# Optimization experiments

Measured on AMD Instinct MI355X. Metric: run time of the kernel, lower is better.

## Reference

```python
import jax, jax.numpy as jnp
import numpy as np

D_MODEL = 768
NUM_HEADS = 12
D_K = D_MODEL // NUM_HEADS


def setup_inputs() -> dict:
    key = jax.random.key(0)
    ks = jax.random.split(key, 11)
    B, S = 2, 2048
    scale = 1.0 / np.sqrt(D_MODEL)
    inp = {
        'query': jax.random.normal(ks[0], (B, S, D_MODEL), jnp.float32),
        'key': jax.random.normal(ks[1], (B, S, D_MODEL), jnp.float32),
        'value': jax.random.normal(ks[2], (B, S, D_MODEL), jnp.float32),
        # Linear params (torch nn.Linear: y = x @ W.T + b); store as [in,out]
        'Wq': jax.random.normal(ks[3], (D_MODEL, D_MODEL), jnp.float32) * scale,
        'bq': jnp.zeros((D_MODEL,), jnp.float32),
        'Wk': jax.random.normal(ks[4], (D_MODEL, D_MODEL), jnp.float32) * scale,
        'bk': jnp.zeros((D_MODEL,), jnp.float32),
        'Wv': jax.random.normal(ks[5], (D_MODEL, D_MODEL), jnp.float32) * scale,
        'bv': jnp.zeros((D_MODEL,), jnp.float32),
        'Wo': jax.random.normal(ks[6], (D_MODEL, D_MODEL), jnp.float32) * scale,
        'bo': jnp.zeros((D_MODEL,), jnp.float32),
    }
    return inp


def _split_heads(x):
    B, S, _ = x.shape
    return x.reshape(B, S, NUM_HEADS, D_K).transpose(0, 2, 1, 3)  # [B,H,S,d_k]


def reference(query, key, value, Wq, bq, Wk, bk, Wv, bv, Wo, bo):
    q = _split_heads(query @ Wq + bq)
    k = _split_heads(key @ Wk + bk)
    v = _split_heads(value @ Wv + bv)
    scores = jnp.einsum('bhqd,bhkd->bhqk', q, k) / np.sqrt(D_K)  # [B,H,S,S]
    attn = jax.nn.softmax(scores, axis=-1)
    x = jnp.einsum('bhqk,bhkd->bhqd', attn, v)  # [B,H,S,d_k]
    B, H, S, _ = x.shape
    x = x.transpose(0, 2, 1, 3).reshape(B, S, D_MODEL)
    return x @ Wo + bo
```

## Files before the change

kernel.cpp:

```cpp
#include <hip/hip_runtime.h>
#include <hip/hip_bf16.h>

#define DM     768
#define HEADS  12
#define DK     64
#define SQ     2048
#define BATCH  2
#define ROWS   4096
#define KTILES 24

typedef __attribute__((ext_vector_type(4))) float f32x4;
typedef __bf16 bf16x8 __attribute__((ext_vector_type(8)));
typedef unsigned short u16x8 __attribute__((ext_vector_type(8)));

#define QSCALE 0.180336880f

static __device__ __forceinline__ unsigned short f2bf(float f) {
    union { float f; unsigned u; } v; v.f = f;
    unsigned u = v.u;
    unsigned lsb = (u >> 16) & 1u;
    u += 0x7fffu + lsb;
    return (unsigned short)(u >> 16);
}

static __device__ __forceinline__ unsigned pack_bf16(float a, float b) {
    __hip_bfloat162 h = __float22bfloat162_rn(make_float2(a, b));
    unsigned u;
    __builtin_memcpy(&u, &h, 4);
    return u;
}

static __device__ __forceinline__ float fexp2(float x) {
#if __has_builtin(__builtin_amdgcn_exp2f)
    return __builtin_amdgcn_exp2f(x);
#else
    return exp2f(x);
#endif
}

static __device__ __forceinline__ bf16x8 load_bf16x8(const unsigned short* p) {
    u16x8 u = *(const u16x8*)p;
    return __builtin_bit_cast(bf16x8, u);
}

static __device__ __forceinline__ void gld_lds16(const unsigned short* g, unsigned short* l) {
    __builtin_amdgcn_global_load_lds((const __attribute__((address_space(1))) void*)g,
                                     (__attribute__((address_space(3))) void*)l,
                                     16, 0, 0);
}

static __device__ __forceinline__ void drain_dma() {
    asm volatile("s_waitcnt vmcnt(0)" ::: "memory");
}

__global__ __launch_bounds__(256) void cvt_frag3(const float* __restrict__ X0,
                                                 const float* __restrict__ X1,
                                                 const float* __restrict__ X2,
                                                 unsigned short* __restrict__ A0,
                                                 unsigned short* __restrict__ A1,
                                                 unsigned short* __restrict__ A2) {
    int z = blockIdx.z;
    const float* X = z == 0 ? X0 : z == 1 ? X1 : X2;
    unsigned short* A = z == 0 ? A0 : z == 1 ? A1 : A2;
    int p = blockIdx.x * 256 + threadIdx.x;
    int lane = p & 63;
    int g = p >> 6;
    int ks = g % KTILES;
    int mt = g / KTILES;
    int row = mt * 16 + (lane & 15);
    int k   = ks * 32 + (lane >> 4) * 8;
    const float* src = X + (size_t)row * DM + k;
    float4 v0 = *(const float4*)src;
    float4 v1 = *(const float4*)(src + 4);
    u16x8 o;
    o[0]=f2bf(v0.x); o[1]=f2bf(v0.y); o[2]=f2bf(v0.z); o[3]=f2bf(v0.w);
    o[4]=f2bf(v1.x); o[5]=f2bf(v1.y); o[6]=f2bf(v1.z); o[7]=f2bf(v1.w);
    *(u16x8*)(A + (size_t)p * 8) = o;
}

__global__ __launch_bounds__(256) void wt_frag4(const float* __restrict__ W0,
                                                const float* __restrict__ W1,
                                                const float* __restrict__ W2,
                                                const float* __restrict__ W3,
                                                unsigned short* __restrict__ F0,
                                                unsigned short* __restrict__ F1,
                                                unsigned short* __restrict__ F2,
                                                unsigned short* __restrict__ F3) {
    int z = blockIdx.z;
    const float* W = z == 0 ? W0 : z == 1 ? W1 : z == 2 ? W2 : W3;
    unsigned short* F = z == 0 ? F0 : z == 1 ? F1 : z == 2 ? F2 : F3;
    int p = blockIdx.x * 256 + threadIdx.x;
    int lane = p & 63;
    int t = (p >> 6) & 3;
    int g = p >> 8;
    int ks = g % KTILES;
    int nb = g / KTILES;
    int n = nb * 64 + t * 16 + (lane & 15);
    int k = ks * 32 + (lane >> 4) * 8;
    u16x8 o;
#pragma unroll
    for (int j = 0; j < 8; ++j) o[j] = f2bf(W[(size_t)(k + j) * DM + n]);
    *(u16x8*)(F + (size_t)p * 8) = o;
}

__global__ __launch_bounds__(256) void gemm_qkv(const unsigned short* __restrict__ A0,
                                                const unsigned short* __restrict__ A1,
                                                const unsigned short* __restrict__ A2,
                                                const unsigned short* __restrict__ F0,
                                                const unsigned short* __restrict__ F1,
                                                const unsigned short* __restrict__ F2,
                                                const float* __restrict__ b0,
                                                const float* __restrict__ b1,
                                                const float* __restrict__ b2,
                                                unsigned short* __restrict__ Qo,
                                                unsigned short* __restrict__ Ko,
                                                unsigned short* __restrict__ Vo) {
    __shared__ __align__(16) unsigned short ldsB[2][8192];

    int z = blockIdx.z;
    const unsigned short* A = z == 0 ? A0 : z == 1 ? A1 : A2;
    const unsigned short* F = z == 0 ? F0 : z == 1 ? F1 : F2;
    const float* bias        = z == 0 ? b0 : z == 1 ? b1 : b2;

    int w    = threadIdx.x >> 6;
    int lane = threadIdx.x & 63;
    int l15  = lane & 15;
    int quad = lane >> 4;
    int m0 = blockIdx.y * 128 + w * 32;
    int nb = blockIdx.x;
    int mt0 = m0 >> 4;

    const unsigned short* Ap = A + (size_t)mt0 * KTILES * 512 + lane * 8;
    const unsigned short* Bsrc = F + (size_t)nb * KTILES * 4 * 512 + w * 2048 + lane * 8;
    unsigned short* Bdst = &ldsB[0][w * 2048];

    f32x4 acc[2][4];
#pragma unroll
    for (int i = 0; i < 2; ++i)
#pragma unroll
        for (int t = 0; t < 4; ++t) acc[i][t] = (f32x4){0.f, 0.f, 0.f, 0.f};

#define BSTAGE(buf, c) do { \
        _Pragma("unroll") \
        for (int j = 0; j < 4; ++j) \
            gld_lds16(Bsrc + (size_t)(c) * 8192 + j * 512, Bdst + (buf) * 8192 + j * 512); \
    } while (0)

    BSTAGE(0, 0);

    bf16x8 a_cur[2][4];
#pragma unroll
    for (int k4 = 0; k4 < 4; ++k4)
#pragma unroll
        for (int i = 0; i < 2; ++i)
            a_cur[i][k4] = load_bf16x8(Ap + ((size_t)i * KTILES + k4) * 512);

    for (int c = 0; c < 6; ++c) {
        drain_dma();
        __syncthreads();
        if (c < 5) BSTAGE((c + 1) & 1, c + 1);
        const unsigned short* Bl = &ldsB[c & 1][0];
#pragma unroll
        for (int k4 = 0; k4 < 4; ++k4) {
#pragma unroll
            for (int t = 0; t < 4; ++t) {
                bf16x8 bb = load_bf16x8(Bl + (k4 * 4 + t) * 512 + lane * 8);
#pragma unroll
                for (int i = 0; i < 2; ++i)
                    acc[i][t] = __builtin_amdgcn_mfma_f32_16x16x32_bf16(a_cur[i][k4], bb, acc[i][t], 0, 0, 0);
            }
            if (c < 5) {
#pragma unroll
                for (int i = 0; i < 2; ++i)
                    a_cur[i][k4] = load_bf16x8(Ap + ((size_t)i * KTILES + (c + 1) * 4 + k4) * 512);
            }
        }
    }
#undef BSTAGE

    float scale = (z == 0) ? QSCALE : 1.0f;
#pragma unroll
    for (int t = 0; t < 4; ++t) {
        int col = nb * 64 + t * 16 + l15;
        float bv = bias[col];
        int h = col >> 6, d = col & (DK - 1);
#pragma unroll
        for (int i = 0; i < 2; ++i)
#pragma unroll
            for (int r = 0; r < 4; ++r) {
                int row = m0 + i * 16 + quad * 4 + r;
                float v = (acc[i][t][r] + bv) * scale;
                int bb = row >> 11, s = row & (SQ - 1);
                size_t bh = (size_t)(bb * HEADS + h);
                if (z == 0) {
                    Qo[(bh * SQ + s) * DK + d] = f2bf(v);
                } else if (z == 1) {
                    int sc = s & 63;
                    Ko[(bh * (SQ / 64) + (s >> 6)) * 4096 + sc * 64 +
                       (((d >> 3) ^ ((sc >> 1) & 7)) << 3) + (d & 7)] = f2bf(v);
                } else {
                    int sc = s & 63;
                    Vo[(bh * (SQ / 64) + (s >> 6)) * 4096 + d * 64 +
                       (((sc >> 3) ^ ((d >> 1) & 7)) << 3) + (sc & 7)] = f2bf(v);
                }
            }
    }
}

__global__ __launch_bounds__(256) void flash_attn(const unsigned short* __restrict__ Q,
                                                  const unsigned short* __restrict__ Kb,
                                                  const unsigned short* __restrict__ Vb,
                                                  unsigned short* __restrict__ Af) {
    __shared__ __align__(16) unsigned short ldsK[2][4096];
    __shared__ __align__(16) unsigned short ldsV[2][4096];
    __shared__ __align__(16) unsigned short ldsP[4][32 * 72];

    int w    = threadIdx.x >> 6;
    int lane = threadIdx.x & 63;
    int l15  = lane & 15;
    int quad = lane >> 4;
    int rg   = w >> 1;
    int par  = w & 1;
    int b = blockIdx.z, h = blockIdx.y;
    int q0 = blockIdx.x * 64 + rg * 32;

    size_t bh = (size_t)(b * HEADS + h);
    const unsigned short* Qp = Q  + (bh * SQ + q0) * DK;
    const unsigned short* KB = Kb + bh * (SQ / 64) * 4096;
    const unsigned short* VB = Vb + bh * (SQ / 64) * 4096;

    bf16x8 aq[2][2];
#pragma unroll
    for (int i = 0; i < 2; ++i) {
        aq[i][0] = load_bf16x8(Qp + (i * 16 + l15) * DK + quad * 8);
        aq[i][1] = load_bf16x8(Qp + (i * 16 + l15) * DK + 32 + quad * 8);
    }

    f32x4 o[2][4];
#pragma unroll
    for (int i = 0; i < 2; ++i)
#pragma unroll
        for (int t = 0; t < 4; ++t) o[i][t] = (f32x4){0.f, 0.f, 0.f, 0.f};
    float lsum[2][4] = {{0.f,0.f,0.f,0.f},{0.f,0.f,0.f,0.f}};

    unsigned short* Pw = &ldsP[w][0];

    int koff[4][2], voff[4][2];
#pragma unroll
    for (int t = 0; t < 4; ++t) {
        int pr = (t >> 1) * 32 + 2 * l15 + (t & 1);
        int sw = l15 & 7;
        koff[t][0] = pr * 64 + (((quad)     ^ sw) << 3);
        koff[t][1] = pr * 64 + (((4 + quad) ^ sw) << 3);
        int d = t * 16 + l15;
        int swv = (l15 >> 1) & 7;
        voff[t][0] = d * 64 + (((quad)     ^ swv) << 3);
        voff[t][1] = d * 64 + (((4 + quad) ^ swv) << 3);
    }

    const unsigned short* ksrc = KB + rg * 2048 + lane * 8;
    const unsigned short* vsrc = VB + rg * 2048 + lane * 8;
    unsigned short* kdst = &ldsK[par][rg * 2048 + lane * 8];
    unsigned short* vdst = &ldsV[par][rg * 2048 + lane * 8];

    u16x8 kreg[4], vreg[4];
#define STAGE_LOAD(n) do { \
        _Pragma("unroll") \
        for (int j = 0; j < 4; ++j) { \
            kreg[j] = *(const u16x8*)(ksrc + (size_t)(n) * 4096 + j * 512); \
            vreg[j] = *(const u16x8*)(vsrc + (size_t)(n) * 4096 + j * 512); \
        } \
    } while (0)
#define STAGE_WRITE() do { \
        _Pragma("unroll") \
        for (int j = 0; j < 4; ++j) { \
            *(u16x8*)(kdst + j * 512) = kreg[j]; \
            *(u16x8*)(vdst + j * 512) = vreg[j]; \
        } \
    } while (0)

    STAGE_LOAD(par);
    STAGE_WRITE();

    const unsigned short* Kl = &ldsK[par][0];
    const unsigned short* Vl = &ldsV[par][0];

    for (int s = 0; s < 16; ++s) {
        __syncthreads();

        if (s < 15) STAGE_LOAD(2 * s + 2 + par);

        f32x4 sc[2][4];
#pragma unroll
        for (int i = 0; i < 2; ++i)
#pragma unroll
            for (int t = 0; t < 4; ++t) sc[i][t] = (f32x4){0.f, 0.f, 0.f, 0.f};

#pragma unroll
        for (int t = 0; t < 4; ++t) {
            bf16x8 k0 = load_bf16x8(Kl + koff[t][0]);
            bf16x8 k1 = load_bf16x8(Kl + koff[t][1]);
#pragma unroll
            for (int i = 0; i < 2; ++i) {
                sc[i][t] = __builtin_amdgcn_mfma_f32_16x16x32_bf16(aq[i][0], k0, sc[i][t], 0, 0, 0);
                sc[i][t] = __builtin_amdgcn_mfma_f32_16x16x32_bf16(aq[i][1], k1, sc[i][t], 0, 0, 0);
            }
        }

#pragma unroll
        for (int i = 0; i < 2; ++i)
#pragma unroll
            for (int sub = 0; sub < 2; ++sub)
#pragma unroll
                for (int r = 0; r < 4; ++r) {
                    float e0 = fexp2(sc[i][2 * sub][r]);
                    float e1 = fexp2(sc[i][2 * sub + 1][r]);
                    lsum[i][r] += e0 + e1;
                    *(unsigned*)(Pw + (i * 16 + quad * 4 + r) * 72 + sub * 32 + l15 * 2)
                        = pack_bf16(e0, e1);
                }

        bf16x8 pf[2][2];
#pragma unroll
        for (int i = 0; i < 2; ++i) {
            pf[i][0] = load_bf16x8(Pw + (i * 16 + l15) * 72 + quad * 8);
            pf[i][1] = load_bf16x8(Pw + (i * 16 + l15) * 72 + 32 + quad * 8);
        }

#pragma unroll
        for (int t = 0; t < 4; ++t) {
            bf16x8 v0 = load_bf16x8(Vl + voff[t][0]);
            bf16x8 v1 = load_bf16x8(Vl + voff[t][1]);
#pragma unroll
            for (int i = 0; i < 2; ++i) {
                o[i][t] = __builtin_amdgcn_mfma_f32_16x16x32_bf16(pf[i][0], v0, o[i][t], 0, 0, 0);
                o[i][t] = __builtin_amdgcn_mfma_f32_16x16x32_bf16(pf[i][1], v1, o[i][t], 0, 0, 0);
            }
        }

        __syncthreads();
        if (s < 15) STAGE_WRITE();
    }
#undef STAGE_LOAD
#undef STAGE_WRITE

    float* fO = (float*)&ldsK[0][0];
    float* fL = (float*)&ldsV[0][0];
    if (par == 1) {
#pragma unroll
        for (int i = 0; i < 2; ++i)
#pragma unroll
            for (int r = 0; r < 4; ++r) {
                int rowin = i * 16 + quad * 4 + r;
#pragma unroll
                for (int t = 0; t < 4; ++t)
                    fO[rg * 2048 + rowin * 64 + t * 16 + l15] = o[i][t][r];
                fL[rg * 512 + rowin * 16 + l15] = lsum[i][r];
            }
    }
    __syncthreads();
    if (par == 0) {
#pragma unroll
        for (int i = 0; i < 2; ++i)
#pragma unroll
            for (int r = 0; r < 4; ++r) {
                int rowin = i * 16 + quad * 4 + r;
                float l = lsum[i][r] + fL[rg * 512 + rowin * 16 + l15];
                l += __shfl_xor(l, 1);
                l += __shfl_xor(l, 2);
                l += __shfl_xor(l, 4);
                l += __shfl_xor(l, 8);
                float inv = 1.0f / l;
                int R  = b * SQ + q0 + rowin;
                int mt = R >> 4;
#pragma unroll
                for (int t = 0; t < 4; ++t) {
                    float val = o[i][t][r] + fO[rg * 2048 + rowin * 64 + t * 16 + l15];
                    int ks    = h * 2 + (t >> 1);
                    int quadp = ((t & 1) << 1) + (l15 >> 3);
                    int j     = l15 & 7;
                    Af[(size_t)(mt * KTILES + ks) * 512 +
                       (size_t)((quadp << 4) + (rowin & 15)) * 8 + j] = f2bf(val * inv);
                }
            }
    }
}

__global__ __launch_bounds__(256) void gemm_out(const unsigned short* __restrict__ Af,
                                                const unsigned short* __restrict__ Ff,
                                                const float* __restrict__ bias,
                                                float* __restrict__ out) {
    __shared__ __align__(16) unsigned short ldsB[2][8192];

    int w    = threadIdx.x >> 6;
    int lane = threadIdx.x & 63;
    int l15  = lane & 15;
    int quad = lane >> 4;
    int m0 = blockIdx.y * 64 + w * 16;
    int nb = blockIdx.x;
    int mt = m0 >> 4;

    const unsigned short* Ap = Af + (size_t)mt * KTILES * 512 + lane * 8;
    const unsigned short* Bsrc = Ff + (size_t)nb * KTILES * 4 * 512 + w * 2048 + lane * 8;
    unsigned short* Bdst = &ldsB[0][w * 2048];

    f32x4 acc[4];
#pragma unroll
    for (int t = 0; t < 4; ++t) acc[t] = (f32x4){0.f, 0.f, 0.f, 0.f};

#define BSTAGE(buf, c) do { \
        _Pragma("unroll") \
        for (int j = 0; j < 4; ++j) \
            gld_lds16(Bsrc + (size_t)(c) * 8192 + j * 512, Bdst + (buf) * 8192 + j * 512); \
    } while (0)

    BSTAGE(0, 0);

    bf16x8 a_cur[4];
#pragma unroll
    for (int k4 = 0; k4 < 4; ++k4)
        a_cur[k4] = load_bf16x8(Ap + (size_t)k4 * 512);

    for (int c = 0; c < 6; ++c) {
        drain_dma();
        __syncthreads();
        if (c < 5) BSTAGE((c + 1) & 1, c + 1);
        const unsigned short* Bl = &ldsB[c & 1][0];
#pragma unroll
        for (int k4 = 0; k4 < 4; ++k4) {
#pragma unroll
            for (int t = 0; t < 4; ++t) {
                bf16x8 bb = load_bf16x8(Bl + (k4 * 4 + t) * 512 + lane * 8);
                acc[t] = __builtin_amdgcn_mfma_f32_16x16x32_bf16(a_cur[k4], bb, acc[t], 0, 0, 0);
            }
            if (c < 5)
                a_cur[k4] = load_bf16x8(Ap + (size_t)((c + 1) * 4 + k4) * 512);
        }
    }
#undef BSTAGE

#pragma unroll
    for (int t = 0; t < 4; ++t) {
        int col = nb * 64 + t * 16 + l15;
        float bv = bias[col];
#pragma unroll
        for (int r = 0; r < 4; ++r) {
            int row = m0 + quad * 4 + r;
            out[(size_t)row * DM + col] = acc[t][r] + bv;
        }
    }
}

extern "C" void kernel_launch(void* const* d_in, const int* in_sizes, int n_in,
                              void* d_out, int out_size, void* d_ws, size_t ws_size,
                              hipStream_t stream) {
    const float* query = (const float*)d_in[0];
    const float* key   = (const float*)d_in[1];
    const float* value = (const float*)d_in[2];
    const float* Wq = (const float*)d_in[3];  const float* bq = (const float*)d_in[4];
    const float* Wk = (const float*)d_in[5];  const float* bk = (const float*)d_in[6];
    const float* Wv = (const float*)d_in[7];  const float* bv = (const float*)d_in[8];
    const float* Wo = (const float*)d_in[9];  const float* bo = (const float*)d_in[10];

    const size_t NX = (size_t)ROWS * DM;
    const size_t NW = (size_t)DM * DM;
    unsigned short* Xq  = (unsigned short*)d_ws;
    unsigned short* Xk  = Xq  + NX;
    unsigned short* Xv  = Xk  + NX;
    unsigned short* Qb  = Xv  + NX;
    unsigned short* Kb  = Qb  + NX;
    unsigned short* Vt  = Kb  + NX;
    unsigned short* Wtq = Vt  + NX;
    unsigned short* Wtk = Wtq + NW;
    unsigned short* Wtv = Wtk + NW;
    unsigned short* Wto = Wtv + NW;

    cvt_frag3<<<dim3((unsigned)(NX / 8 / 256), 1, 3), 256, 0, stream>>>(
        query, key, value, Xq, Xk, Xv);

    wt_frag4<<<dim3((unsigned)(NW / 8 / 256), 1, 4), 256, 0, stream>>>(
        Wq, Wk, Wv, Wo, Wtq, Wtk, Wtv, Wto);

    gemm_qkv<<<dim3(DM / 64, ROWS / 128, 3), 256, 0, stream>>>(
        Xq, Xk, Xv, Wtq, Wtk, Wtv, bq, bk, bv, Qb, Kb, Vt);

    flash_attn<<<dim3(SQ / 64, HEADS, BATCH), 256, 0, stream>>>(Qb, Kb, Vt, Xq);

    gemm_out<<<dim3(DM / 64, ROWS / 64), 256, 0, stream>>>(Xq, Wto, bo, (float*)d_out);
}
```

Measured before the change: 199.4 us.

## Load K/V fragments directly from global into registers, drop LDS staging and barriers

The flash attention kernel no longer stages K and V tiles through shared memory. Each wave now loads its MFMA operand fragments straight from global memory into registers using the pre-swizzled layout, prefetching the next tile after each MFMA phase. This removes the per-iteration __syncthreads and the LDS write/read traffic, and adds s_setprio around the MFMA blocks. The grid is also flattened and remapped so that consecutive blocks spread across heads, which may change how L2 is shared. The cost is redundant global/L2 reads, since both wave pairs that share a row group now fetch the same K/V data, plus higher register pressure from 16 extra vector registers.

```diff
diff --git a/kernel.cpp b/kernel.cpp
--- a/kernel.cpp
+++ b/kernel.cpp
@@ -211,9 +211,9 @@
                                                   const unsigned short* __restrict__ Kb,
                                                   const unsigned short* __restrict__ Vb,
                                                   unsigned short* __restrict__ Af) {
-    __shared__ __align__(16) unsigned short ldsK[2][4096];
-    __shared__ __align__(16) unsigned short ldsV[2][4096];
     __shared__ __align__(16) unsigned short ldsP[4][32 * 72];
+    __shared__ __align__(16) float fO[2][2048];
+    __shared__ __align__(16) float fL[2][512];
 
     int w    = threadIdx.x >> 6;
     int lane = threadIdx.x & 63;
@@ -221,8 +221,12 @@
     int quad = lane >> 4;
     int rg   = w >> 1;
     int par  = w & 1;
-    int b = blockIdx.z, h = blockIdx.y;
-    int q0 = blockIdx.x * 64 + rg * 32;
+
+    int lin  = blockIdx.x;
+    int nlin = (lin & 7) * 96 + (lin >> 3);
+    int q0   = (nlin & 31) * 64 + rg * 32;
+    int h    = (nlin >> 5) % HEADS;
+    int b    = nlin / (32 * HEADS);
 
     size_t bh = (size_t)(b * HEADS + h);
     const unsigned short* Qp = Q  + (bh * SQ + q0) * DK;
@@ -258,54 +262,48 @@
         voff[t][1] = d * 64 + (((4 + quad) ^ swv) << 3);
     }
 
-    const unsigned short* ksrc = KB + rg * 2048 + lane * 8;
-    const unsigned short* vsrc = VB + rg * 2048 + lane * 8;
-    unsigned short* kdst = &ldsK[par][rg * 2048 + lane * 8];
-    unsigned short* vdst = &ldsV[par][rg * 2048 + lane * 8];
-
-    u16x8 kreg[4], vreg[4];
-#define STAGE_LOAD(n) do { \
+    u16x8 kreg[8], vreg[8];
+#define LOADK(n) do { \
+        const unsigned short* kc_ = KB + (size_t)(n) * 4096; \
         _Pragma("unroll") \
-        for (int j = 0; j < 4; ++j) { \
-            kreg[j] = *(const u16x8*)(ksrc + (size_t)(n) * 4096 + j * 512); \
-            vreg[j] = *(const u16x8*)(vsrc + (size_t)(n) * 4096 + j * 512); \
+        for (int t = 0; t < 4; ++t) { \
+            kreg[2 * t]     = *(const u16x8*)(kc_ + koff[t][0]); \
+            kreg[2 * t + 1] = *(const u16x8*)(kc_ + koff[t][1]); \
         } \
     } while (0)
-#define STAGE_WRITE() do { \
+#define LOADV(n) do { \
+        const unsigned short* vc_ = VB + (size_t)(n) * 4096; \
         _Pragma("unroll") \
-        for (int j = 0; j < 4; ++j) { \
-            *(u16x8*)(kdst + j * 512) = kreg[j]; \
-            *(u16x8*)(vdst + j * 512) = vreg[j]; \
+        for (int t = 0; t < 4; ++t) { \
+            vreg[2 * t]     = *(const u16x8*)(vc_ + voff[t][0]); \
+            vreg[2 * t + 1] = *(const u16x8*)(vc_ + voff[t][1]); \
         } \
     } while (0)
 
-    STAGE_LOAD(par);
-    STAGE_WRITE();
-
-    const unsigned short* Kl = &ldsK[par][0];
-    const unsigned short* Vl = &ldsV[par][0];
+    LOADK(par);
+    LOADV(par);
 
     for (int s = 0; s < 16; ++s) {
-        __syncthreads();
-
-        if (s < 15) STAGE_LOAD(2 * s + 2 + par);
-
         f32x4 sc[2][4];
 #pragma unroll
         for (int i = 0; i < 2; ++i)
 #pragma unroll
             for (int t = 0; t < 4; ++t) sc[i][t] = (f32x4){0.f, 0.f, 0.f, 0.f};
 
+        __builtin_amdgcn_s_setprio(1);
 #pragma unroll
         for (int t = 0; t < 4; ++t) {
-            bf16x8 k0 = load_bf16x8(Kl + koff[t][0]);
-            bf16x8 k1 = load_bf16x8(Kl + koff[t][1]);
+            bf16x8 k0 = __builtin_bit_cast(bf16x8, kreg[2 * t]);
+            bf16x8 k1 = __builtin_bit_cast(bf16x8, kreg[2 * t + 1]);
 #pragma unroll
             for (int i = 0; i < 2; ++i) {
                 sc[i][t] = __builtin_amdgcn_mfma_f32_16x16x32_bf16(aq[i][0], k0, sc[i][t], 0, 0, 0);
                 sc[i][t] = __builtin_amdgcn_mfma_f32_16x16x32_bf16(aq[i][1], k1, sc[i][t], 0, 0, 0);
             }
         }
+        __builtin_amdgcn_s_setprio(0);
+
+        if (s < 15) LOADK(2 * s + 2 + par);
 
 #pragma unroll
         for (int i = 0; i < 2; ++i)
@@ -327,25 +325,24 @@
             pf[i][1] = load_bf16x8(Pw + (i * 16 + l15) * 72 + 32 + quad * 8);
         }
 
+        __builtin_amdgcn_s_setprio(1);
 #pragma unroll
         for (int t = 0; t < 4; ++t) {
-            bf16x8 v0 = load_bf16x8(Vl + voff[t][0]);
-            bf16x8 v1 = load_bf16x8(Vl + voff[t][1]);
+            bf16x8 v0 = __builtin_bit_cast(bf16x8, vreg[2 * t]);
+            bf16x8 v1 = __builtin_bit_cast(bf16x8, vreg[2 * t + 1]);
 #pragma unroll
             for (int i = 0; i < 2; ++i) {
                 o[i][t] = __builtin_amdgcn_mfma_f32_16x16x32_bf16(pf[i][0], v0, o[i][t], 0, 0, 0);
                 o[i][t] = __builtin_amdgcn_mfma_f32_16x16x32_bf16(pf[i][1], v1, o[i][t], 0, 0, 0);
             }
         }
-
-        __syncthreads();
-        if (s < 15) STAGE_WRITE();
-    }
-#undef STAGE_LOAD
-#undef STAGE_WRITE
-
-    float* fO = (float*)&ldsK[0][0];
-    float* fL = (float*)&ldsV[0][0];
+        __builtin_amdgcn_s_setprio(0);
+
+        if (s < 15) LOADV(2 * s + 2 + par);
+    }
+#undef LOADK
+#undef LOADV
+
     if (par == 1) {
 #pragma unroll
         for (int i = 0; i < 2; ++i)
@@ -354,8 +351,8 @@
                 int rowin = i * 16 + quad * 4 + r;
 #pragma unroll
                 for (int t = 0; t < 4; ++t)
-                    fO[rg * 2048 + rowin * 64 + t * 16 + l15] = o[i][t][r];
-                fL[rg * 512 + rowin * 16 + l15] = lsum[i][r];
+                    fO[rg][rowin * 64 + t * 16 + l15] = o[i][t][r];
+                fL[rg][rowin * 16 + l15] = lsum[i][r];
             }
     }
     __syncthreads();
@@ -365,7 +362,7 @@
 #pragma unroll
             for (int r = 0; r < 4; ++r) {
                 int rowin = i * 16 + quad * 4 + r;
-                float l = lsum[i][r] + fL[rg * 512 + rowin * 16 + l15];
+                float l = lsum[i][r] + fL[rg][rowin * 16 + l15];
                 l += __shfl_xor(l, 1);
                 l += __shfl_xor(l, 2);
                 l += __shfl_xor(l, 4);
@@ -375,7 +372,7 @@
                 int mt = R >> 4;
 #pragma unroll
                 for (int t = 0; t < 4; ++t) {
-                    float val = o[i][t][r] + fO[rg * 2048 + rowin * 64 + t * 16 + l15];
+                    float val = o[i][t][r] + fO[rg][rowin * 64 + t * 16 + l15];
                     int ks    = h * 2 + (t >> 1);
                     int quadp = ((t & 1) << 1) + (l15 >> 3);
                     int j     = l15 & 7;
@@ -484,7 +481,7 @@
     gemm_qkv<<<dim3(DM / 64, ROWS / 128, 3), 256, 0, stream>>>(
         Xq, Xk, Xv, Wtq, Wtk, Wtv, bq, bk, bv, Qb, Kb, Vt);
 
-    flash_attn<<<dim3(SQ / 64, HEADS, BATCH), 256, 0, stream>>>(Qb, Kb, Vt, Xq);
+    flash_attn<<<dim3((SQ / 64) * HEADS * BATCH, 1, 1), 256, 0, stream>>>(Qb, Kb, Vt, Xq);
 
     gemm_out<<<dim3(DM / 64, ROWS / 64), 256, 0, stream>>>(Xq, Wto, bo, (float*)d_out);
 }
```

Result: no change. 201.8 us (+1.2%).
